# Performance work log

Hardware: AMD Instinct MI355X
Metric: run time of the kernel (lower is better)

## Reference

```python
import jax, jax.numpy as jnp
import numpy as np

H = 256   # hidden_size
B = 64    # batch_size
LP = 2048 # passage length
LQ = 64   # question length


def _linear(x, W, b):
    # torch nn.Linear: y = x @ W.T + b
    return jnp.matmul(x, W.T) + b


def _gru_cell(x, h, w_ih, w_hh, b_ih, b_hh):
    # torch GRUCell semantics: x is input, h is hidden state
    gi = jnp.matmul(x, w_ih.T) + b_ih   # [B, 3*2H]
    gh = jnp.matmul(h, w_hh.T) + b_hh
    i_r, i_z, i_n = jnp.split(gi, 3, axis=-1)
    h_r, h_z, h_n = jnp.split(gh, 3, axis=-1)
    r = jax.nn.sigmoid(i_r + h_r)
    z = jax.nn.sigmoid(i_z + h_z)
    n = jnp.tanh(i_n + r * h_n)
    return (1.0 - z) * n + z * h


def setup_inputs() -> dict:
    key = jax.random.key(0)
    ks = jax.random.split(key, 17)
    s = lambda i, shape: jax.random.normal(ks[i], shape, dtype=jnp.float32) * 0.05
    return {
        "passEnc": jax.random.normal(ks[0], (LP, B, 2 * H), dtype=jnp.float32),
        "quesEnc": jax.random.normal(ks[1], (LQ, B, 2 * H), dtype=jnp.float32),
        "WQu_W": s(2, (H, 2 * H)), "WQu_b": s(3, (H,)),
        "WQv_W": s(4, (H, H)),     "WQv_b": s(5, (H,)),
        "WPh_W": s(6, (H, 2 * H)), "WPh_b": s(7, (H,)),
        "Wah_W": s(8, (H, 2 * H)), "Wah_b": s(9, (H,)),
        "Vt1": s(10, (B, H, 1)),
        "Vt2": s(11, (B, H, 1)),
        "VQr": s(12, (1, 1, H)),
        "gru_wih": s(13, (6 * H, 2 * H)), "gru_whh": s(14, (6 * H, 2 * H)),
        "gru_bih": s(15, (6 * H,)),       "gru_bhh": s(16, (6 * H,)),
    }


def reference(passEnc, quesEnc, WQu_W, WQu_b, WQv_W, WQv_b, WPh_W, WPh_b,
              Wah_W, Wah_b, Vt1, Vt2, VQr, gru_wih, gru_whh, gru_bih, gru_bhh):
    # --- question-aware initial state rQ ---
    # temp: [lQ, B, H] (VQr path broadcasts over lQ and B)
    temp = jnp.tanh(_linear(quesEnc, WQu_W, WQu_b) + _linear(VQr, WQv_W, WQv_b))
    sQ = jnp.einsum('qbh,bh->bq', temp, Vt1[..., 0])          # [B, lQ]
    a = jax.nn.softmax(sQ, axis=1)
    rQ = jnp.einsum('bq,qbd->bd', a, quesEnc)                 # [B, 2H]

    passP = _linear(passEnc, WPh_W, WPh_b)                    # [lP, B, H], reused both steps

    def pointer_step(rQ):
        temp2 = jnp.tanh(passP + _linear(rQ, Wah_W, Wah_b))   # [lP, B, H]
        sP = jnp.einsum('pbh,bh->bp', temp2, Vt2[..., 0])     # [B, lP]
        aP = jax.nn.softmax(sP, axis=1)
        ct = jnp.einsum('bp,pbd->bd', aP, passEnc)            # [B, 2H]
        return aP, ct

    aP1, ct = pointer_step(rQ)
    rQ = _gru_cell(rQ, ct, gru_wih, gru_whh, gru_bih, gru_bhh)
    aP2, _ = pointer_step(rQ)
    return (aP1, aP2)


if __name__ == "__main__":
    out = reference(**setup_inputs())
    print(out[0].shape, out[1].shape)
```

## Files before the change

### kernel.cpp

```cpp
#include <hip/hip_runtime.h>
#include <math.h>


constexpr int Bn   = 64;
constexpr int Hn   = 256;
constexpr int D2H  = 512;
constexpr int LPn  = 2048;
constexpr int LQn  = 64;

typedef __attribute__((ext_vector_type(8))) short bf16x8;
typedef __attribute__((ext_vector_type(4))) float f32x4;

typedef const __attribute__((address_space(1))) unsigned int* gup;
typedef __attribute__((address_space(3))) unsigned int* lup;
__device__ inline void async16(const void* g, void* l) {
  __builtin_amdgcn_global_load_lds((gup)g, (lup)l, 16, 0, 0);
}

__device__ inline float waveAllSum(float v) {
  #pragma unroll
  for (int o = 32; o > 0; o >>= 1) v += __shfl_xor(v, o, 64);
  return v;
}
__device__ inline float waveAllMax(float v) {
  #pragma unroll
  for (int o = 32; o > 0; o >>= 1) v = fmaxf(v, __shfl_xor(v, o, 64));
  return v;
}

__device__ inline short f2bf_rtne(float f) {
  union { float f; unsigned u; } v; v.f = f;
  unsigned r = v.u + 0x7FFF + ((v.u >> 16) & 1);
  return (short)(r >> 16);
}
__device__ inline unsigned pk2(float lo, float hi) {
  union { float f; unsigned u; } a, b; a.f = lo; b.f = hi;
  return __builtin_amdgcn_perm(b.u + 0x8000u, a.u + 0x8000u, 0x07060302u);
}
__device__ inline bf16x8 cvt8(f32x4 a0, f32x4 a1) {
  union { unsigned u[4]; bf16x8 v; } r;
  r.u[0] = pk2(a0[0], a0[1]);
  r.u[1] = pk2(a0[2], a0[3]);
  r.u[2] = pk2(a1[0], a1[1]);
  r.u[3] = pk2(a1[2], a1[3]);
  return r.v;
}

__global__ __launch_bounds__(256) void k_wcvt(const float* __restrict__ WQu,
                                              const float* __restrict__ WPh,
                                              short* __restrict__ q16,
                                              short* __restrict__ p16) {
  int e = (blockIdx.x * 256 + threadIdx.x) * 4;
  const float* src; short* dst; int off;
  if (e < 131072) { src = WQu; dst = q16; off = e; }
  else            { src = WPh; dst = p16; off = e - 131072; }
  f32x4 f = *(const f32x4*)&src[off];
  short4 h;
  h.x = f2bf_rtne(f[0]); h.y = f2bf_rtne(f[1]);
  h.z = f2bf_rtne(f[2]); h.w = f2bf_rtne(f[3]);
  *(short4*)&dst[off] = h;
}

__global__ __launch_bounds__(256) void k_v2(const float* __restrict__ VQr,
                                            const float* __restrict__ WQv_W,
                                            const float* __restrict__ WQv_b,
                                            float* __restrict__ v2) {
  __shared__ float s[256];
  int t = threadIdx.x;
  s[t] = VQr[t];
  __syncthreads();
  float acc = WQv_b[t];
  for (int k = 0; k < 256; ++k) acc += s[k] * WQv_W[t * 256 + k];
  v2[t] = acc;
}

__global__ __launch_bounds__(256, 3) void k_mfma(
    const float* __restrict__ A,
    const short* __restrict__ Wb,
    const float* __restrict__ bias,
    const float* __restrict__ u,
    const float* __restrict__ vt,
    short* __restrict__ pp,
    float* __restrict__ sOut,
    int ustride, int sstride)
{
  __shared__ union {
    struct { float As[128 * 64]; short Bs[128 * 64]; } m;
    float sred[256];
  } sm;
  const int t = threadIdx.x;
  const int w = t >> 6, l = t & 63, l15 = l & 15, quad = l >> 4;
  const int wm = w >> 1, wn = w & 1;
  const long bm = (long)blockIdx.x * 128;
  const int n0 = blockIdx.y * 128;

  f32x4 acc[4][4];
  #pragma unroll
  for (int i = 0; i < 4; ++i)
    #pragma unroll
    for (int j = 0; j < 4; ++j)
      acc[i][j] = (f32x4)0.f;

  const float* gA = A + (bm + (t >> 4)) * 512 + (((t & 15) ^ (t >> 4)) << 2);
  const short* gB = Wb + (size_t)(n0 + (t >> 3)) * 512 + (((t & 7) ^ ((t >> 3) & 7)) << 3);
  float* lA = sm.m.As + t * 4;
  short* lB = sm.m.Bs + t * 8;

  for (int k0 = 0; k0 < 512; k0 += 64) {
    #pragma unroll
    for (int it = 0; it < 8; ++it)
      async16(gA + it * 8192 + k0, lA + it * 1024);
    #pragma unroll
    for (int it = 0; it < 4; ++it)
      async16(gB + it * 16384 + k0, lB + it * 2048);
    __syncthreads();
    #pragma unroll
    for (int ks = 0; ks < 2; ++ks) {
      bf16x8 af[4], bfv[4];
      const int cA = ks * 8 + quad * 2;
      const int cB = ks * 4 + quad;
      #pragma unroll
      for (int i = 0; i < 4; ++i) {
        const int R = wm * 64 + i * 16 + l15;
        const float* base = &sm.m.As[R * 64];
        f32x4 p0 = *(const f32x4*)(base + ((cA ^ l15) << 2));
        f32x4 p1 = *(const f32x4*)(base + (((cA + 1) ^ l15) << 2));
        af[i] = cvt8(p0, p1);
      }
      #pragma unroll
      for (int j = 0; j < 4; ++j) {
        const int R = wn * 64 + j * 16 + l15;
        bfv[j] = *(const bf16x8*)&sm.m.Bs[R * 64 + ((cB ^ (l15 & 7)) << 3)];
      }
      #pragma unroll
      for (int i = 0; i < 4; ++i)
        #pragma unroll
        for (int j = 0; j < 4; ++j)
          acc[i][j] = __builtin_amdgcn_mfma_f32_16x16x32_bf16(af[i], bfv[j], acc[i][j], 0, 0, 0);
    }
    __syncthreads();
  }

  short* ppt = pp ? pp + ((size_t)(blockIdx.x * 2 + blockIdx.y) * 256 + t) * 64 : nullptr;
  float srow[4][4];
  #pragma unroll
  for (int i = 0; i < 4; ++i) {
    #pragma unroll
    for (int r = 0; r < 4; ++r) srow[i][r] = 0.f;
    unsigned pk[8];
    const int bb = i * 16 + quad * 4;
    #pragma unroll
    for (int j = 0; j < 4; ++j) {
      const int n = n0 + wn * 64 + j * 16 + l15;
      const float bn = bias[n];
      float v0 = acc[i][j][0] + bn, v1 = acc[i][j][1] + bn;
      float v2 = acc[i][j][2] + bn, v3 = acc[i][j][3] + bn;
      if (ppt) { pk[j * 2] = pk2(v0, v1); pk[j * 2 + 1] = pk2(v2, v3); }
      srow[i][0] += tanhf(v0 + u[ustride * (bb + 0) + n]) * vt[(bb + 0) * 256 + n];
      srow[i][1] += tanhf(v1 + u[ustride * (bb + 1) + n]) * vt[(bb + 1) * 256 + n];
      srow[i][2] += tanhf(v2 + u[ustride * (bb + 2) + n]) * vt[(bb + 2) * 256 + n];
      srow[i][3] += tanhf(v3 + u[ustride * (bb + 3) + n]) * vt[(bb + 3) * 256 + n];
    }
    if (ppt) {
      uint4 s0 = {pk[0], pk[1], pk[2], pk[3]};
      uint4 s1 = {pk[4], pk[5], pk[6], pk[7]};
      *(uint4*)&ppt[i * 16] = s0;
      *(uint4*)&ppt[i * 16 + 8] = s1;
    }
  }
  #pragma unroll
  for (int off = 1; off < 16; off <<= 1)
    #pragma unroll
    for (int i = 0; i < 4; ++i)
      #pragma unroll
      for (int r = 0; r < 4; ++r)
        srow[i][r] += __shfl_xor(srow[i][r], off, 64);
  if (l15 == 0)
    #pragma unroll
    for (int i = 0; i < 4; ++i)
      #pragma unroll
      for (int r = 0; r < 4; ++r)
        sm.sred[wn * 128 + wm * 64 + i * 16 + quad * 4 + r] = srow[i][r];
  __syncthreads();
  if (t < 128) {
    float s = sm.sred[t] + sm.sred[128 + t];
    int b = t & 63;
    int pg = blockIdx.x * 2 + (t >> 6);
    atomicAdd(&sOut[(size_t)b * sstride + pg], s);
  }
}

__global__ __launch_bounds__(256) void k_sp2(const short* __restrict__ pp,
                                             const float* __restrict__ u2,
                                             const float* __restrict__ vt,
                                             float* __restrict__ sP) {
  __shared__ float sred[256];
  const int g = blockIdx.x, t = threadIdx.x;
  const int w = t >> 6, l = t & 63, l15 = l & 15, quad = l >> 4;
  const int wm = w >> 1, wn = w & 1;
  const int n0 = (g & 1) * 128;
  const short* src = pp + ((size_t)g * 256 + t) * 64;
  float srow[4][4];
  #pragma unroll
  for (int i = 0; i < 4; ++i) {
    uint4 q0 = *(const uint4*)&src[i * 16];
    uint4 q1 = *(const uint4*)&src[i * 16 + 8];
    unsigned pk[8] = {q0.x, q0.y, q0.z, q0.w, q1.x, q1.y, q1.z, q1.w};
    #pragma unroll
    for (int r = 0; r < 4; ++r) srow[i][r] = 0.f;
    const int bb = i * 16 + quad * 4;
    #pragma unroll
    for (int j = 0; j < 4; ++j) {
      const int n = n0 + wn * 64 + j * 16 + l15;
      #pragma unroll
      for (int r = 0; r < 4; ++r) {
        unsigned word = pk[j * 2 + (r >> 1)];
        unsigned bits = (r & 1) ? (word & 0xFFFF0000u) : (word << 16);
        float val = __uint_as_float(bits);
        srow[i][r] += tanhf(val + u2[(bb + r) * 256 + n]) * vt[(bb + r) * 256 + n];
      }
    }
  }
  #pragma unroll
  for (int off = 1; off < 16; off <<= 1)
    #pragma unroll
    for (int i = 0; i < 4; ++i)
      #pragma unroll
      for (int r = 0; r < 4; ++r)
        srow[i][r] += __shfl_xor(srow[i][r], off, 64);
  if (l15 == 0)
    #pragma unroll
    for (int i = 0; i < 4; ++i)
      #pragma unroll
      for (int r = 0; r < 4; ++r)
        sred[wn * 128 + wm * 64 + i * 16 + quad * 4 + r] = srow[i][r];
  __syncthreads();
  if (t < 128) {
    float s = sred[t] + sred[128 + t];
    int b = t & 63;
    int pg = (g >> 1) * 2 + (t >> 6);
    atomicAdd(&sP[(size_t)b * LPn + pg], s);
  }
}

__global__ __launch_bounds__(256) void k_rq_u1(const float* __restrict__ sQ,
                                               const float* __restrict__ quesEnc,
                                               const float* __restrict__ Wah,
                                               const float* __restrict__ Wah_b,
                                               float* __restrict__ rQ,
                                               float* __restrict__ u1) {
  int b = blockIdx.x, tid = threadIdx.x;
  __shared__ float s_a[LQn];
  __shared__ float s_r[D2H];
  if (tid < 64) {
    float s = sQ[b * LQn + tid];
    float m = waveAllMax(s);
    float e = expf(s - m);
    float sum = waveAllSum(e);
    s_a[tid] = e / sum;
  }
  __syncthreads();
  #pragma unroll
  for (int rep = 0; rep < 2; ++rep) {
    int d = tid + rep * 256;
    float acc = 0.f;
    for (int q = 0; q < LQn; ++q)
      acc += s_a[q] * quesEnc[(size_t)(q * Bn + b) * D2H + d];
    s_r[d] = acc;
    rQ[b * D2H + d] = acc;
  }
  __syncthreads();
  float accu = Wah_b[tid];
  const float* wr = Wah + (size_t)tid * 512;
  for (int k4 = 0; k4 < 128; ++k4) {
    f32x4 wv = *(const f32x4*)&wr[k4 * 4];
    f32x4 rv = *(const f32x4*)&s_r[k4 * 4];
    accu += wv[0] * rv[0] + wv[1] * rv[1] + wv[2] * rv[2] + wv[3] * rv[3];
  }
  u1[b * Hn + tid] = accu;
}

__global__ __launch_bounds__(256) void k_softmax(const float* __restrict__ sP,
                                                 float* __restrict__ out) {
  int b = blockIdx.x, tid = threadIdx.x;
  int lane = tid & 63, wid = tid >> 6;
  __shared__ float red[4];
  float v[8];
  float m = -1e30f;
  #pragma unroll
  for (int i = 0; i < 8; ++i) {
    v[i] = sP[b * LPn + i * 256 + tid];
    m = fmaxf(m, v[i]);
  }
  m = waveAllMax(m);
  if (lane == 0) red[wid] = m;
  __syncthreads();
  m = fmaxf(fmaxf(red[0], red[1]), fmaxf(red[2], red[3]));
  float s = 0.f;
  #pragma unroll
  for (int i = 0; i < 8; ++i) { v[i] = expf(v[i] - m); s += v[i]; }
  s = waveAllSum(s);
  __syncthreads();
  if (lane == 0) red[wid] = s;
  __syncthreads();
  s = red[0] + red[1] + red[2] + red[3];
  float inv = 1.0f / s;
  #pragma unroll
  for (int i = 0; i < 8; ++i) out[b * LPn + i * 256 + tid] = v[i] * inv;
}

__global__ __launch_bounds__(256) void k_ct(const float* __restrict__ aP,
                                            const float* __restrict__ passEnc,
                                            float* __restrict__ ct) {
  int b = blockIdx.x, pc = blockIdx.y, tid = threadIdx.x;
  int dg = tid & 127;
  int pg = tid >> 7;
  f32x4 acc = (f32x4)0.f;
  #pragma unroll
  for (int pp = 0; pp < 32; ++pp) {
    int p = pc * 64 + pg * 32 + pp;
    float a = aP[b * LPn + p];
    acc += a * *(const f32x4*)&passEnc[((size_t)p * Bn + b) * D2H + dg * 4];
  }
  __shared__ f32x4 sacc[256];
  sacc[tid] = acc;
  __syncthreads();
  if (pg == 0) {
    acc += sacc[tid + 128];
    float* dst = &ct[b * D2H + dg * 4];
    atomicAdd(dst + 0, acc[0]);
    atomicAdd(dst + 1, acc[1]);
    atomicAdd(dst + 2, acc[2]);
    atomicAdd(dst + 3, acc[3]);
  }
}

__global__ __launch_bounds__(256) void k_gih(const float* __restrict__ rQ,
                                             const float* __restrict__ ct,
                                             const float* __restrict__ wih,
                                             const float* __restrict__ whh,
                                             const float* __restrict__ bih,
                                             const float* __restrict__ bhh,
                                             float* __restrict__ gi,
                                             float* __restrict__ gh) {
  __shared__ float sw[16 * 512];
  int blk = blockIdx.x;
  bool isH = blk >= 96;
  const float* W = isH ? whh : wih;
  const float* X = isH ? ct : rQ;
  const float* bias = isH ? bhh : bih;
  float* G = isH ? gh : gi;
  int r0 = (isH ? blk - 96 : blk) * 16;
  int t = threadIdx.x;
  #pragma unroll
  for (int it = 0; it < 8; ++it) {
    int f4 = it * 256 + t;
    *(f32x4*)&sw[f4 * 4] = *(const f32x4*)&W[(size_t)r0 * 512 + f4 * 4];
  }
  __syncthreads();
  int b = t & 63;
  int rbase = (t >> 6) * 4;
  const float* x = X + b * 512;
  float acc[4];
  #pragma unroll
  for (int oo = 0; oo < 4; ++oo) acc[oo] = bias[r0 + rbase + oo];
  for (int k4 = 0; k4 < 128; ++k4) {
    f32x4 xv = *(const f32x4*)&x[k4 * 4];
    #pragma unroll
    for (int oo = 0; oo < 4; ++oo) {
      f32x4 wv = *(const f32x4*)&sw[(rbase + oo) * 512 + k4 * 4];
      acc[oo] += wv[0] * xv[0] + wv[1] * xv[1] + wv[2] * xv[2] + wv[3] * xv[3];
    }
  }
  #pragma unroll
  for (int oo = 0; oo < 4; ++oo)
    G[b * 1536 + r0 + rbase + oo] = acc[oo];
}

__global__ __launch_bounds__(256) void k_gates(const float* __restrict__ gi,
                                               const float* __restrict__ gh,
                                               const float* __restrict__ ct,
                                               float* __restrict__ rQ2) {
  int idx = blockIdx.x * 256 + threadIdx.x;
  int b = idx >> 9;
  int j = idx & 511;
  const float* gib = gi + b * 1536;
  const float* ghb = gh + b * 1536;
  float r = 1.f / (1.f + expf(-(gib[j] + ghb[j])));
  float z = 1.f / (1.f + expf(-(gib[512 + j] + ghb[512 + j])));
  float n = tanhf(gib[1024 + j] + r * ghb[1024 + j]);
  rQ2[b * D2H + j] = (1.f - z) * n + z * ct[b * D2H + j];
}

__global__ __launch_bounds__(256) void k_u2(const float* __restrict__ rQ2,
                                            const float* __restrict__ Wah,
                                            const float* __restrict__ Wah_b,
                                            float* __restrict__ u2) {
  int m = blockIdx.x, n = threadIdx.x;
  __shared__ float s_r[D2H];
  s_r[n]       = rQ2[m * D2H + n];
  s_r[n + 256] = rQ2[m * D2H + n + 256];
  __syncthreads();
  float acc = Wah_b[n];
  const float* wr = Wah + (size_t)n * 512;
  for (int k4 = 0; k4 < 128; ++k4) {
    f32x4 wv = *(const f32x4*)&wr[k4 * 4];
    f32x4 rv = *(const f32x4*)&s_r[k4 * 4];
    acc += wv[0] * rv[0] + wv[1] * rv[1] + wv[2] * rv[2] + wv[3] * rv[3];
  }
  u2[m * Hn + n] = acc;
}

extern "C" void kernel_launch(void* const* d_in, const int* in_sizes, int n_in,
                              void* d_out, int out_size, void* d_ws, size_t ws_size,
                              hipStream_t stream) {
  const float* passEnc  = (const float*)d_in[0];
  const float* quesEnc  = (const float*)d_in[1];
  const float* WQu_W    = (const float*)d_in[2];
  const float* WQu_b    = (const float*)d_in[3];
  const float* WQv_W    = (const float*)d_in[4];
  const float* WQv_b    = (const float*)d_in[5];
  const float* WPh_W    = (const float*)d_in[6];
  const float* WPh_b    = (const float*)d_in[7];
  const float* Wah_W    = (const float*)d_in[8];
  const float* Wah_b    = (const float*)d_in[9];
  const float* Vt1      = (const float*)d_in[10];
  const float* Vt2      = (const float*)d_in[11];
  const float* VQr      = (const float*)d_in[12];
  const float* gru_wih  = (const float*)d_in[13];
  const float* gru_whh  = (const float*)d_in[14];
  const float* gru_bih  = (const float*)d_in[15];
  const float* gru_bhh  = (const float*)d_in[16];
  float* out = (float*)d_out;

  float* ws = (float*)d_ws;
  float* v2    = ws;
  float* rQ    = v2 + 256;
  float* u1    = rQ + 32768;
  float* u2    = u1 + 16384;
  float* sP    = u2 + 16384;
  float* ct    = sP + 131072;
  float* gi    = ct + 32768;
  float* gh    = gi + 98304;
  float* rQ2   = gh + 98304;
  float* sQ    = rQ2 + 32768;
  short* wqu16 = (short*)(sQ + 4096);
  short* wph16 = wqu16 + 131072;
  short* pp16  = wph16 + 131072;

  hipMemsetAsync(sQ, 0, Bn * LQn * sizeof(float), stream);
  hipMemsetAsync(sP, 0, Bn * LPn * sizeof(float), stream);
  hipMemsetAsync(ct, 0, Bn * D2H * sizeof(float), stream);

  k_wcvt<<<256, 256, 0, stream>>>(WQu_W, WPh_W, wqu16, wph16);
  k_v2<<<1, 256, 0, stream>>>(VQr, WQv_W, WQv_b, v2);

  k_mfma<<<dim3(LQn * Bn / 128, 2), 256, 0, stream>>>(
      quesEnc, wqu16, WQu_b, v2, Vt1, nullptr, sQ, 0, LQn);
  k_rq_u1<<<Bn, 256, 0, stream>>>(sQ, quesEnc, Wah_W, Wah_b, rQ, u1);

  k_mfma<<<dim3(LPn * Bn / 128, 2), 256, 0, stream>>>(
      passEnc, wph16, WPh_b, u1, Vt2, pp16, sP, Hn, LPn);
  k_softmax<<<Bn, 256, 0, stream>>>(sP, out);

  k_ct<<<dim3(Bn, 32), 256, 0, stream>>>(out, passEnc, ct);

  k_gih<<<192, 256, 0, stream>>>(rQ, ct, gru_wih, gru_whh, gru_bih, gru_bhh, gi, gh);
  k_gates<<<Bn * D2H / 256, 256, 0, stream>>>(gi, gh, ct, rQ2);
  k_u2<<<Bn, 256, 0, stream>>>(rQ2, Wah_W, Wah_b, u2);

  hipMemsetAsync(sP, 0, Bn * LPn * sizeof(float), stream);
  k_sp2<<<LPn * Bn / 64, 256, 0, stream>>>(pp16, u2, Vt2, sP);
  k_softmax<<<Bn, 256, 0, stream>>>(sP, out + Bn * LPn);
}
```

Baseline: 825.5 us.

## Convert A tile to bf16 on load, swap grid axes, coalesce pp layout

The GEMM kernel now loads the fp32 A tile into registers and converts it to bf16 before writing to LDS, rather than async-copying fp32 into LDS and converting at every fragment read. This halves the A tile's LDS footprint and lets launch bounds allow 4 blocks per CU. The grid axes are swapped so the two N-halves sharing one A row-block run next to each other, which should improve L2 reuse of passEnc. The bf16 pp intermediate is relaid so each wave's stores and loads are contiguous, and the reader kernel is updated to match. The trade-off is that A loads become synchronous through registers and no longer overlap with the async B copy.

```diff
diff --git a/kernel.cpp b/kernel.cpp
--- a/kernel.cpp
+++ b/kernel.cpp
@@ -74,7 +74,7 @@
   v2[t] = acc;
 }
 
-__global__ __launch_bounds__(256, 3) void k_mfma(
+__global__ __launch_bounds__(256, 4) void k_mfma(
     const float* __restrict__ A,
     const short* __restrict__ Wb,
     const float* __restrict__ bias,
@@ -85,14 +85,14 @@
     int ustride, int sstride)
 {
   __shared__ union {
-    struct { float As[128 * 64]; short Bs[128 * 64]; } m;
+    struct { short As[128 * 64]; short Bs[128 * 64]; } m;
     float sred[256];
   } sm;
   const int t = threadIdx.x;
   const int w = t >> 6, l = t & 63, l15 = l & 15, quad = l >> 4;
   const int wm = w >> 1, wn = w & 1;
-  const long bm = (long)blockIdx.x * 128;
-  const int n0 = blockIdx.y * 128;
+  const long bm = (long)blockIdx.y * 128;
+  const int n0 = blockIdx.x * 128;
 
   f32x4 acc[4][4];
   #pragma unroll
@@ -101,36 +101,40 @@
     for (int j = 0; j < 4; ++j)
       acc[i][j] = (f32x4)0.f;
 
-  const float* gA = A + (bm + (t >> 4)) * 512 + (((t & 15) ^ (t >> 4)) << 2);
   const short* gB = Wb + (size_t)(n0 + (t >> 3)) * 512 + (((t & 7) ^ ((t >> 3) & 7)) << 3);
-  float* lA = sm.m.As + t * 4;
   short* lB = sm.m.Bs + t * 8;
 
   for (int k0 = 0; k0 < 512; k0 += 64) {
-    #pragma unroll
-    for (int it = 0; it < 8; ++it)
-      async16(gA + it * 8192 + k0, lA + it * 1024);
     #pragma unroll
     for (int it = 0; it < 4; ++it)
       async16(gB + it * 16384 + k0, lB + it * 2048);
+    f32x4 a0[4], a1[4];
+    #pragma unroll
+    for (int s = 0; s < 4; ++s) {
+      const int e = s * 256 + t, row = e >> 3, c = e & 7;
+      const float* g = A + (bm + row) * 512 + k0 + (c << 3);
+      a0[s] = *(const f32x4*)g;
+      a1[s] = *(const f32x4*)(g + 4);
+    }
+    #pragma unroll
+    for (int s = 0; s < 4; ++s) {
+      const int e = s * 256 + t, row = e >> 3, c = e & 7;
+      *(bf16x8*)&sm.m.As[row * 64 + ((c ^ (row & 7)) << 3)] = cvt8(a0[s], a1[s]);
+    }
     __syncthreads();
     #pragma unroll
     for (int ks = 0; ks < 2; ++ks) {
       bf16x8 af[4], bfv[4];
-      const int cA = ks * 8 + quad * 2;
-      const int cB = ks * 4 + quad;
+      const int cc = ks * 4 + quad;
       #pragma unroll
       for (int i = 0; i < 4; ++i) {
         const int R = wm * 64 + i * 16 + l15;
-        const float* base = &sm.m.As[R * 64];
-        f32x4 p0 = *(const f32x4*)(base + ((cA ^ l15) << 2));
-        f32x4 p1 = *(const f32x4*)(base + (((cA + 1) ^ l15) << 2));
-        af[i] = cvt8(p0, p1);
+        af[i] = *(const bf16x8*)&sm.m.As[R * 64 + ((cc ^ (l15 & 7)) << 3)];
       }
       #pragma unroll
       for (int j = 0; j < 4; ++j) {
         const int R = wn * 64 + j * 16 + l15;
-        bfv[j] = *(const bf16x8*)&sm.m.Bs[R * 64 + ((cB ^ (l15 & 7)) << 3)];
+        bfv[j] = *(const bf16x8*)&sm.m.Bs[R * 64 + ((cc ^ (l15 & 7)) << 3)];
       }
       #pragma unroll
       for (int i = 0; i < 4; ++i)
@@ -141,7 +145,8 @@
     __syncthreads();
   }
 
-  short* ppt = pp ? pp + ((size_t)(blockIdx.x * 2 + blockIdx.y) * 256 + t) * 64 : nullptr;
+  short* ppt = pp ? pp + (((size_t)blockIdx.y * 2 + blockIdx.x) * 16384 + (size_t)w * 4096 + l * 8)
+                  : nullptr;
   float srow[4][4];
   #pragma unroll
   for (int i = 0; i < 4; ++i) {
@@ -164,8 +169,8 @@
     if (ppt) {
       uint4 s0 = {pk[0], pk[1], pk[2], pk[3]};
       uint4 s1 = {pk[4], pk[5], pk[6], pk[7]};
-      *(uint4*)&ppt[i * 16] = s0;
-      *(uint4*)&ppt[i * 16 + 8] = s1;
+      *(uint4*)&ppt[i * 1024]       = s0;
+      *(uint4*)&ppt[i * 1024 + 512] = s1;
     }
   }
   #pragma unroll
@@ -185,7 +190,7 @@
   if (t < 128) {
     float s = sm.sred[t] + sm.sred[128 + t];
     int b = t & 63;
-    int pg = blockIdx.x * 2 + (t >> 6);
+    int pg = blockIdx.y * 2 + (t >> 6);
     atomicAdd(&sOut[(size_t)b * sstride + pg], s);
   }
 }
@@ -199,12 +204,12 @@
   const int w = t >> 6, l = t & 63, l15 = l & 15, quad = l >> 4;
   const int wm = w >> 1, wn = w & 1;
   const int n0 = (g & 1) * 128;
-  const short* src = pp + ((size_t)g * 256 + t) * 64;
+  const short* src = pp + (size_t)g * 16384 + (size_t)w * 4096 + l * 8;
   float srow[4][4];
   #pragma unroll
   for (int i = 0; i < 4; ++i) {
-    uint4 q0 = *(const uint4*)&src[i * 16];
-    uint4 q1 = *(const uint4*)&src[i * 16 + 8];
+    uint4 q0 = *(const uint4*)&src[i * 1024];
+    uint4 q1 = *(const uint4*)&src[i * 1024 + 512];
     unsigned pk[8] = {q0.x, q0.y, q0.z, q0.w, q1.x, q1.y, q1.z, q1.w};
     #pragma unroll
     for (int r = 0; r < 4; ++r) srow[i][r] = 0.f;
@@ -455,11 +460,11 @@
   k_wcvt<<<256, 256, 0, stream>>>(WQu_W, WPh_W, wqu16, wph16);
   k_v2<<<1, 256, 0, stream>>>(VQr, WQv_W, WQv_b, v2);
 
-  k_mfma<<<dim3(LQn * Bn / 128, 2), 256, 0, stream>>>(
+  k_mfma<<<dim3(2, LQn * Bn / 128), 256, 0, stream>>>(
       quesEnc, wqu16, WQu_b, v2, Vt1, nullptr, sQ, 0, LQn);
   k_rq_u1<<<Bn, 256, 0, stream>>>(sQ, quesEnc, Wah_W, Wah_b, rQ, u1);
 
-  k_mfma<<<dim3(LPn * Bn / 128, 2), 256, 0, stream>>>(
+  k_mfma<<<dim3(2, LPn * Bn / 128), 256, 0, stream>>>(
       passEnc, wph16, WPh_b, u1, Vt2, pp16, sP, Hn, LPn);
   k_softmax<<<Bn, 256, 0, stream>>>(sP, out);
 
```

Result: slower. 922.2 us (+11.7%).
